# Optimization experiments

Hardware: AMD Instinct MI355X
Metric: run time of the kernel (lower is better)

## Reference

```python
import jax, jax.numpy as jnp
import numpy as np

N_NODES = 50000
N_EDGES = 800000
IN_FEATS = 256
OUT_FEATS = 128


def setup_inputs() -> dict:
    key = jax.random.key(0)
    k1, k2, k3, k4 = jax.random.split(key, 4)
    feat = jax.random.normal(k1, (N_NODES, IN_FEATS), dtype=jnp.float32)
    # xavier uniform init for weight [in, out]
    limit = float(np.sqrt(6.0 / (IN_FEATS + OUT_FEATS)))
    weight = jax.random.uniform(k2, (IN_FEATS, OUT_FEATS), minval=-limit, maxval=limit, dtype=jnp.float32)
    bias = jnp.zeros((OUT_FEATS,), dtype=jnp.float32)
    src = jax.random.randint(k3, (N_EDGES,), 0, N_NODES, dtype=jnp.int32)
    dst = jax.random.randint(k4, (N_EDGES,), 0, N_NODES, dtype=jnp.int32)
    return {"feat": feat, "weight": weight, "bias": bias, "src": src, "dst": dst}


def reference(feat, weight, bias, src, dst):
    N = feat.shape[0]
    in_f, out_f = weight.shape
    # right normalization: 1 / out_degree(src node), clamped to >= 1
    deg = jax.ops.segment_sum(jnp.ones(src.shape[0], dtype=feat.dtype), src, num_segments=N)
    norm = (1.0 / jnp.maximum(deg, 1.0))[:, None]  # [N,1]
    if in_f > out_f:
        # transform first (cheaper messages), then normalize + aggregate
        h = jnp.matmul(feat, weight) * norm          # [N, out]
        rst = jax.ops.segment_sum(h[src], dst, num_segments=N)  # scatter-sum over edges
    else:
        h = feat * norm                               # [N, in]
        rst = jax.ops.segment_sum(h[src], dst, num_segments=N)
        rst = jnp.matmul(rst, weight)
    return rst + bias
```

## Files before the change

kernel.cpp:

```cpp
#include <hip/hip_runtime.h>

#define N_NODES 50000
#define N_EDGES 800000
#define IN_F 256
#define OUT_F 128

#define CHUNKS 128
#define EPC (N_EDGES / CHUNKS)
#define BINW (N_NODES / 4)
#define NWORDS (N_NODES / 4)
#define RGB 196
#define HIST_BLOCKS (2 * CHUNKS)
#define CPW (CHUNKS / 4)

#define GEMM_START HIST_BLOCKS
#define GEMMF_BLOCKS 196
#define SCAT_BLOCKS 782

typedef __attribute__((ext_vector_type(8))) short short8;
typedef __attribute__((ext_vector_type(4))) float float4_t;

__device__ __forceinline__ short f2bf(float f) {
  unsigned u = __builtin_bit_cast(unsigned, f);
  u = u + 0x7FFFu + ((u >> 16) & 1u);
  return (short)(u >> 16);
}

__device__ __forceinline__ float bflo(unsigned u) {
  return __builtin_bit_cast(float, u << 16);
}
__device__ __forceinline__ float bfhi(unsigned u) {
  return __builtin_bit_cast(float, u & 0xFFFF0000u);
}

__global__ __launch_bounds__(512) void fused1_kernel(const int* __restrict__ src,
                                                     const int* __restrict__ dst,
                                                     unsigned char* __restrict__ pdst8,
                                                     unsigned char* __restrict__ psrc8,
                                                     unsigned char* __restrict__ rank8,
                                                     const float* __restrict__ W,
                                                     const float* __restrict__ feat,
                                                     unsigned short* __restrict__ h,
                                                     int* __restrict__ cursor) {
  __shared__ uint4 smem4[4096];
  int b = blockIdx.x;
  int tid = threadIdx.x;

  if (b >= GEMM_START) {
    if (b == GEMM_START && tid == 0) *cursor = 0;
    short* wl = (short*)smem4;
#pragma unroll
    for (int i = 0; i < 64; ++i) {
      int idx = i * 512 + tid;
      int k = idx >> 7, n = idx & 127;
      int s = k >> 5, q = (k >> 3) & 3, j = k & 7;
      int tt = n >> 4, m = n & 15;
      wl[((s * 8 + tt) * 64 + q * 16 + m) * 8 + j] = f2bf(W[idx]);
    }
    __syncthreads();

    int w = tid >> 6, l = tid & 63;
    int m = l & 15, q = l >> 4;
    long base = (long)(b - GEMM_START) * 256 + w * 32;

    float4_t acc[2][8];
#pragma unroll
    for (int r = 0; r < 2; ++r)
#pragma unroll
      for (int to = 0; to < 8; ++to) acc[r][to] = (float4_t)(0.0f);

    long row0 = base + m;
    long row1 = base + 16 + m;
    long r0c = row0 < N_NODES - 1 ? row0 : N_NODES - 1;
    long r1c = row1 < N_NODES - 1 ? row1 : N_NODES - 1;
    const float* a0p = feat + (size_t)r0c * IN_F;
    const float* a1p = feat + (size_t)r1c * IN_F;
    const short8* wl8 = (const short8*)smem4;

#pragma unroll
    for (int s = 0; s < 8; ++s) {
      int k0 = s * 32 + q * 8;
      float4_t av0a = *(const float4_t*)(a0p + k0);
      float4_t av0b = *(const float4_t*)(a0p + k0 + 4);
      float4_t av1a = *(const float4_t*)(a1p + k0);
      float4_t av1b = *(const float4_t*)(a1p + k0 + 4);
      short8 fa0, fa1;
#pragma unroll
      for (int i = 0; i < 4; ++i) {
        fa0[i] = f2bf(av0a[i]);
        fa0[i + 4] = f2bf(av0b[i]);
        fa1[i] = f2bf(av1a[i]);
        fa1[i + 4] = f2bf(av1b[i]);
      }
#pragma unroll
      for (int to = 0; to < 8; ++to) {
        short8 fb = wl8[(s * 8 + to) * 64 + l];
        acc[0][to] = __builtin_amdgcn_mfma_f32_16x16x32_bf16(fa0, fb, acc[0][to], 0, 0, 0);
        acc[1][to] = __builtin_amdgcn_mfma_f32_16x16x32_bf16(fa1, fb, acc[1][to], 0, 0, 0);
      }
    }

#pragma unroll
    for (int r = 0; r < 2; ++r) {
#pragma unroll
      for (int i = 0; i < 4; ++i) {
        long row = base + r * 16 + q * 4 + i;
        if (row < N_NODES) {
          size_t ho = (size_t)row * OUT_F;
#pragma unroll
          for (int to = 0; to < 8; ++to) {
            h[ho + to * 16 + m] = (unsigned short)f2bf(acc[r][to][i]);
          }
        }
      }
    }
    return;
  }

  unsigned* bins = (unsigned*)smem4;
  int hs = b >> 7;
  int c = b & 127;
  uint4* b4 = (uint4*)bins;
  for (int j = tid; j < BINW / 4; j += 512) b4[j] = (uint4){0u, 0u, 0u, 0u};
  __syncthreads();
  const int* key = hs ? src : dst;
  int e0 = c * EPC;

  auto process = [&](int v, int eI) {
    unsigned sh = (v & 3) * 8;
    unsigned old = atomicAdd(&bins[v >> 2], 1u << sh);
    if (!hs) rank8[eI] = (unsigned char)((old >> sh) & 0xFFu);
  };

#pragma unroll 2
  for (int tile = 0; tile < 3; ++tile) {
    int i = tile * 2048 + tid;
    int k0 = key[e0 + i];
    int k1 = key[e0 + i + 512];
    int k2 = key[e0 + i + 1024];
    int k3 = key[e0 + i + 1536];
    process(k0, e0 + i);
    process(k1, e0 + i + 512);
    process(k2, e0 + i + 1024);
    process(k3, e0 + i + 1536);
  }
  {
    int i = 6144 + tid;
    if (i < EPC) process(key[e0 + i], e0 + i);
  }
  __syncthreads();
  uint4* p128 = (uint4*)((hs ? psrc8 : pdst8) + (size_t)c * N_NODES);
  const uint4* s128 = (const uint4*)bins;
  for (int j = tid; j < BINW / 4; j += 512) p128[j] = s128[j];
}

__global__ __launch_bounds__(256) void reduceoff_kernel(const unsigned char* __restrict__ pdst8,
                                                        const unsigned char* __restrict__ psrc8,
                                                        unsigned char* __restrict__ delta8,
                                                        int* __restrict__ cnt,
                                                        int* __restrict__ row_start,
                                                        int* __restrict__ cursor,
                                                        float* __restrict__ norm) {
  __shared__ unsigned tot[4][64];
  int g = blockIdx.x, side = blockIdx.y;
  int t = threadIdx.x;
  int w = t >> 6, l = t & 63;
  int wd = g * 64 + l;
  bool ok = wd < NWORDS;
  int wdc = ok ? wd : NWORDS - 1;
  const unsigned* P = (const unsigned*)(side == 0 ? pdst8 : psrc8);

  unsigned vals[CPW];
  unsigned s = 0;
#pragma unroll
  for (int i = 0; i < CPW; ++i) {
    vals[i] = P[(size_t)(w * CPW + i) * NWORDS + wdc];
    s += vals[i];
  }
  tot[w][l] = s;
  __syncthreads();

  if (side == 0) {
    unsigned base = 0;
#pragma unroll
    for (int w2 = 0; w2 < 4; ++w2)
      if (w2 < w) base += tot[w2][l];
    unsigned run = base;
    unsigned* D = (unsigned*)delta8;
    if (ok) {
#pragma unroll
      for (int i = 0; i < CPW; ++i) {
        D[(size_t)(w * CPW + i) * NWORDS + wd] = run;
        run += vals[i];
      }
    }
    if (w == 0) {
      unsigned ftot = tot[0][l] + tot[1][l] + tot[2][l] + tot[3][l];
      if (!ok) ftot = 0;
      int c0 = ftot & 255, c1 = (ftot >> 8) & 255, c2 = (ftot >> 16) & 255, c3 = ftot >> 24;
      int T = c0 + c1 + c2 + c3;
      int x = T;
#pragma unroll
      for (int off = 1; off < 64; off <<= 1) {
        int y = __shfl_up(x, off);
        if (l >= off) x += y;
      }
      int waveTotal = __shfl(x, 63);
      int sb = 0;
      if (l == 63) sb = atomicAdd(cursor, waveTotal);
      sb = __shfl(sb, 63);
      int E = sb + x - T;
      if (ok) {
        int4 cv = {c0, c1, c2, c3};
        int4 rv = {E, E + c0, E + c0 + c1, E + c0 + c1 + c2};
        ((int4*)cnt)[wd] = cv;
        ((int4*)row_start)[wd] = rv;
      }
    }
  } else {
    if (w == 0 && ok) {
      unsigned ftot = tot[0][l] + tot[1][l] + tot[2][l] + tot[3][l];
      float4 nv;
      int d0 = ftot & 255, d1 = (ftot >> 8) & 255, d2 = (ftot >> 16) & 255, d3 = (int)(ftot >> 24);
      nv.x = 1.0f / (float)(d0 > 1 ? d0 : 1);
      nv.y = 1.0f / (float)(d1 > 1 ? d1 : 1);
      nv.z = 1.0f / (float)(d2 > 1 ? d2 : 1);
      nv.w = 1.0f / (float)(d3 > 1 ? d3 : 1);
      ((float4*)norm)[wd] = nv;
    }
  }
}

__global__ __launch_bounds__(256) void scat_kernel(const int* __restrict__ src,
                                                   const int* __restrict__ dst,
                                                   const int* __restrict__ row_start,
                                                   const unsigned char* __restrict__ delta8,
                                                   const unsigned char* __restrict__ rank8,
                                                   int* __restrict__ eidx) {
  int gt = blockIdx.x * 256 + threadIdx.x;
  int e = gt * 4;
  if (e >= N_EDGES) return;
  int4 d4 = *(const int4*)(dst + e);
  int4 s4 = *(const int4*)(src + e);
  unsigned rr = *(const unsigned*)(rank8 + e);
  int dd[4] = {d4.x, d4.y, d4.z, d4.w};
  int ss[4] = {s4.x, s4.y, s4.z, s4.w};
#pragma unroll
  for (int k = 0; k < 4; ++k) {
    int c = (e + k) / EPC;
    int d = dd[k];
    int pos = row_start[d] + (int)delta8[(size_t)c * N_NODES + d] + (int)((rr >> (8 * k)) & 0xFFu);
    eidx[pos] = ss[k];
  }
}

__global__ __launch_bounds__(256) void agg_kernel(const unsigned short* __restrict__ h,
                                                  const int* __restrict__ row_start,
                                                  const int* __restrict__ cnt,
                                                  const int* __restrict__ eidx,
                                                  const float* __restrict__ norm,
                                                  const float* __restrict__ bias,
                                                  float* __restrict__ out) {
  int w = threadIdx.x >> 6, l = threadIdx.x & 63;
  int d = blockIdx.x * 4 + w;
  int rs = row_start[d], re = rs + cnt[d];
  const unsigned* __restrict__ hu = (const unsigned*)h;
  int rowsel = l >> 5, cp = l & 31;
  float a0 = 0.f, a1 = 0.f, a2 = 0.f, a3 = 0.f;
  for (int bse = rs; bse < re; bse += 64) {
    int n = re - bse; if (n > 64) n = 64;
    int e = (l < n) ? eidx[bse + l] : 0;
    int half = (n + 1) >> 1;
    int j = 0;
    for (; j + 4 <= half; j += 4) {
      int i0 = 2 * j + rowsel;
      int s0 = __shfl(e, i0);
      int s1 = __shfl(e, i0 + 2);
      int s2 = __shfl(e, i0 + 4);
      int s3 = __shfl(e, i0 + 6);
      uint2 v0 = *(const uint2*)(hu + (size_t)s0 * 64 + 2 * cp);
      uint2 v1 = *(const uint2*)(hu + (size_t)s1 * 64 + 2 * cp);
      uint2 v2 = *(const uint2*)(hu + (size_t)s2 * 64 + 2 * cp);
      uint2 v3 = *(const uint2*)(hu + (size_t)s3 * 64 + 2 * cp);
      float nm0 = norm[s0], nm1 = norm[s1], nm2 = norm[s2], nm3 = norm[s3];
      if (i0 >= n) { v0.x = 0; v0.y = 0; }
      if (i0 + 2 >= n) { v1.x = 0; v1.y = 0; }
      if (i0 + 4 >= n) { v2.x = 0; v2.y = 0; }
      if (i0 + 6 >= n) { v3.x = 0; v3.y = 0; }
      a0 = fmaf(bflo(v0.x), nm0, a0); a1 = fmaf(bfhi(v0.x), nm0, a1);
      a2 = fmaf(bflo(v0.y), nm0, a2); a3 = fmaf(bfhi(v0.y), nm0, a3);
      a0 = fmaf(bflo(v1.x), nm1, a0); a1 = fmaf(bfhi(v1.x), nm1, a1);
      a2 = fmaf(bflo(v1.y), nm1, a2); a3 = fmaf(bfhi(v1.y), nm1, a3);
      a0 = fmaf(bflo(v2.x), nm2, a0); a1 = fmaf(bfhi(v2.x), nm2, a1);
      a2 = fmaf(bflo(v2.y), nm2, a2); a3 = fmaf(bfhi(v2.y), nm2, a3);
      a0 = fmaf(bflo(v3.x), nm3, a0); a1 = fmaf(bfhi(v3.x), nm3, a1);
      a2 = fmaf(bflo(v3.y), nm3, a2); a3 = fmaf(bfhi(v3.y), nm3, a3);
    }
    for (; j + 2 <= half; j += 2) {
      int i0 = 2 * j + rowsel;
      int i1 = i0 + 2;
      int s0 = __shfl(e, i0);
      int s1 = __shfl(e, i1);
      uint2 v0 = *(const uint2*)(hu + (size_t)s0 * 64 + 2 * cp);
      uint2 v1 = *(const uint2*)(hu + (size_t)s1 * 64 + 2 * cp);
      float nm0 = norm[s0], nm1 = norm[s1];
      if (i0 >= n) { v0.x = 0; v0.y = 0; }
      if (i1 >= n) { v1.x = 0; v1.y = 0; }
      a0 = fmaf(bflo(v0.x), nm0, a0); a1 = fmaf(bfhi(v0.x), nm0, a1);
      a2 = fmaf(bflo(v0.y), nm0, a2); a3 = fmaf(bfhi(v0.y), nm0, a3);
      a0 = fmaf(bflo(v1.x), nm1, a0); a1 = fmaf(bfhi(v1.x), nm1, a1);
      a2 = fmaf(bflo(v1.y), nm1, a2); a3 = fmaf(bfhi(v1.y), nm1, a3);
    }
    for (; j < half; ++j) {
      int i0 = 2 * j + rowsel;
      int s0 = __shfl(e, i0);
      uint2 v0 = *(const uint2*)(hu + (size_t)s0 * 64 + 2 * cp);
      float nm0 = norm[s0];
      if (i0 >= n) { v0.x = 0; v0.y = 0; }
      a0 = fmaf(bflo(v0.x), nm0, a0); a1 = fmaf(bfhi(v0.x), nm0, a1);
      a2 = fmaf(bflo(v0.y), nm0, a2); a3 = fmaf(bfhi(v0.y), nm0, a3);
    }
  }
  a0 += __shfl_xor(a0, 32);
  a1 += __shfl_xor(a1, 32);
  a2 += __shfl_xor(a2, 32);
  a3 += __shfl_xor(a3, 32);
  if (rowsel == 0) {
    float4 bv = ((const float4*)bias)[cp];
    float4 o;
    o.x = a0 + bv.x; o.y = a1 + bv.y; o.z = a2 + bv.z; o.w = a3 + bv.w;
    ((float4*)(out + (size_t)d * OUT_F))[cp] = o;
  }
}

extern "C" void kernel_launch(void* const* d_in, const int* in_sizes, int n_in,
                              void* d_out, int out_size, void* d_ws, size_t ws_size,
                              hipStream_t stream) {
  const float* feat = (const float*)d_in[0];
  const float* weight = (const float*)d_in[1];
  const float* bias = (const float*)d_in[2];
  const int* src = (const int*)d_in[3];
  const int* dst = (const int*)d_in[4];
  float* out = (float*)d_out;

  char* ws = (char*)d_ws;
  size_t off = 0;
  auto alloc = [&](size_t bytes) -> void* {
    void* p = ws + off;
    off += (bytes + 511) & ~(size_t)511;
    return p;
  };
  int* cursor = (int*)alloc(4);
  int* cnt = (int*)alloc(N_NODES * 4);
  int* row_start = (int*)alloc(N_NODES * 4);
  float* norm = (float*)alloc(N_NODES * 4);
  int* eidx = (int*)alloc(N_EDGES * 4);
  unsigned short* h = (unsigned short*)alloc((size_t)N_NODES * OUT_F * 2);
  unsigned char* pdst8 = (unsigned char*)alloc((size_t)CHUNKS * N_NODES);
  unsigned char* psrc8 = (unsigned char*)alloc((size_t)CHUNKS * N_NODES);
  unsigned char* delta8 = (unsigned char*)alloc((size_t)CHUNKS * N_NODES);
  unsigned char* rank8 = (unsigned char*)alloc((size_t)N_EDGES);
  (void)off; (void)ws_size; (void)in_sizes; (void)n_in; (void)out_size;

  hipLaunchKernelGGL(fused1_kernel, dim3(HIST_BLOCKS + GEMMF_BLOCKS), dim3(512), 0, stream,
                     src, dst, pdst8, psrc8, rank8, weight, feat, h, cursor);
  hipLaunchKernelGGL(reduceoff_kernel, dim3(RGB, 2), dim3(256), 0, stream,
                     pdst8, psrc8, delta8, cnt, row_start, cursor, norm);
  hipLaunchKernelGGL(scat_kernel, dim3(SCAT_BLOCKS), dim3(256), 0, stream,
                     src, dst, row_start, delta8, rank8, eidx);
  hipLaunchKernelGGL(agg_kernel, dim3(N_NODES / 4), dim3(256), 0, stream,
                     h, row_start, cnt, eidx, norm, bias, out);
}
```

Baseline: 170.7 us.

## Split aggregation columns across four grid-y blocks per destination node

The aggregation kernel now launches four blocks per group of destination nodes, each handling a quarter of the output columns (32 floats), with 16 lanes per edge row and four edge rows per wave step. The aim is more parallelism and more loads in flight per node. In exchange, each gather becomes a 64-byte segment per source row instead of 128 bytes. Edge indices and norm values are re-read four times, and per-lane loads shrink from 8 to 4 bytes.

```diff
diff --git a/kernel.cpp b/kernel.cpp
--- a/kernel.cpp
+++ b/kernel.cpp
@@ -263,73 +263,56 @@
                                                   float* __restrict__ out) {
   int w = threadIdx.x >> 6, l = threadIdx.x & 63;
   int d = blockIdx.x * 4 + w;
+  int cq = blockIdx.y;
   int rs = row_start[d], re = rs + cnt[d];
   const unsigned* __restrict__ hu = (const unsigned*)h;
-  int rowsel = l >> 5, cp = l & 31;
-  float a0 = 0.f, a1 = 0.f, a2 = 0.f, a3 = 0.f;
+  int rowsel = l >> 4;
+  int cp = l & 15;
+  int cbase = cq * 16;
+  float a0 = 0.f, a1 = 0.f;
   for (int bse = rs; bse < re; bse += 64) {
     int n = re - bse; if (n > 64) n = 64;
     int e = (l < n) ? eidx[bse + l] : 0;
-    int half = (n + 1) >> 1;
+    int quarter = (n + 3) >> 2;
     int j = 0;
-    for (; j + 4 <= half; j += 4) {
-      int i0 = 2 * j + rowsel;
+    for (; j + 4 <= quarter; j += 4) {
+      int i0 = 4 * j + rowsel;
       int s0 = __shfl(e, i0);
-      int s1 = __shfl(e, i0 + 2);
-      int s2 = __shfl(e, i0 + 4);
-      int s3 = __shfl(e, i0 + 6);
-      uint2 v0 = *(const uint2*)(hu + (size_t)s0 * 64 + 2 * cp);
-      uint2 v1 = *(const uint2*)(hu + (size_t)s1 * 64 + 2 * cp);
-      uint2 v2 = *(const uint2*)(hu + (size_t)s2 * 64 + 2 * cp);
-      uint2 v3 = *(const uint2*)(hu + (size_t)s3 * 64 + 2 * cp);
+      int s1 = __shfl(e, i0 + 4);
+      int s2 = __shfl(e, i0 + 8);
+      int s3 = __shfl(e, i0 + 12);
+      unsigned v0 = hu[(size_t)s0 * 64 + cbase + cp];
+      unsigned v1 = hu[(size_t)s1 * 64 + cbase + cp];
+      unsigned v2 = hu[(size_t)s2 * 64 + cbase + cp];
+      unsigned v3 = hu[(size_t)s3 * 64 + cbase + cp];
       float nm0 = norm[s0], nm1 = norm[s1], nm2 = norm[s2], nm3 = norm[s3];
-      if (i0 >= n) { v0.x = 0; v0.y = 0; }
-      if (i0 + 2 >= n) { v1.x = 0; v1.y = 0; }
-      if (i0 + 4 >= n) { v2.x = 0; v2.y = 0; }
-      if (i0 + 6 >= n) { v3.x = 0; v3.y = 0; }
-      a0 = fmaf(bflo(v0.x), nm0, a0); a1 = fmaf(bfhi(v0.x), nm0, a1);
-      a2 = fmaf(bflo(v0.y), nm0, a2); a3 = fmaf(bfhi(v0.y), nm0, a3);
-      a0 = fmaf(bflo(v1.x), nm1, a0); a1 = fmaf(bfhi(v1.x), nm1, a1);
-      a2 = fmaf(bflo(v1.y), nm1, a2); a3 = fmaf(bfhi(v1.y), nm1, a3);
-      a0 = fmaf(bflo(v2.x), nm2, a0); a1 = fmaf(bfhi(v2.x), nm2, a1);
-      a2 = fmaf(bflo(v2.y), nm2, a2); a3 = fmaf(bfhi(v2.y), nm2, a3);
-      a0 = fmaf(bflo(v3.x), nm3, a0); a1 = fmaf(bfhi(v3.x), nm3, a1);
-      a2 = fmaf(bflo(v3.y), nm3, a2); a3 = fmaf(bfhi(v3.y), nm3, a3);
-    }
-    for (; j + 2 <= half; j += 2) {
-      int i0 = 2 * j + rowsel;
-      int i1 = i0 + 2;
+      if (i0 >= n) v0 = 0u;
+      if (i0 + 4 >= n) v1 = 0u;
+      if (i0 + 8 >= n) v2 = 0u;
+      if (i0 + 12 >= n) v3 = 0u;
+      a0 = fmaf(bflo(v0), nm0, a0); a1 = fmaf(bfhi(v0), nm0, a1);
+      a0 = fmaf(bflo(v1), nm1, a0); a1 = fmaf(bfhi(v1), nm1, a1);
+      a0 = fmaf(bflo(v2), nm2, a0); a1 = fmaf(bfhi(v2), nm2, a1);
+      a0 = fmaf(bflo(v3), nm3, a0); a1 = fmaf(bfhi(v3), nm3, a1);
+    }
+    for (; j < quarter; ++j) {
+      int i0 = 4 * j + rowsel;
       int s0 = __shfl(e, i0);
-      int s1 = __shfl(e, i1);
-      uint2 v0 = *(const uint2*)(hu + (size_t)s0 * 64 + 2 * cp);
-      uint2 v1 = *(const uint2*)(hu + (size_t)s1 * 64 + 2 * cp);
-      float nm0 = norm[s0], nm1 = norm[s1];
-      if (i0 >= n) { v0.x = 0; v0.y = 0; }
-      if (i1 >= n) { v1.x = 0; v1.y = 0; }
-      a0 = fmaf(bflo(v0.x), nm0, a0); a1 = fmaf(bfhi(v0.x), nm0, a1);
-      a2 = fmaf(bflo(v0.y), nm0, a2); a3 = fmaf(bfhi(v0.y), nm0, a3);
-      a0 = fmaf(bflo(v1.x), nm1, a0); a1 = fmaf(bfhi(v1.x), nm1, a1);
-      a2 = fmaf(bflo(v1.y), nm1, a2); a3 = fmaf(bfhi(v1.y), nm1, a3);
-    }
-    for (; j < half; ++j) {
-      int i0 = 2 * j + rowsel;
-      int s0 = __shfl(e, i0);
-      uint2 v0 = *(const uint2*)(hu + (size_t)s0 * 64 + 2 * cp);
+      unsigned v0 = hu[(size_t)s0 * 64 + cbase + cp];
       float nm0 = norm[s0];
-      if (i0 >= n) { v0.x = 0; v0.y = 0; }
-      a0 = fmaf(bflo(v0.x), nm0, a0); a1 = fmaf(bfhi(v0.x), nm0, a1);
-      a2 = fmaf(bflo(v0.y), nm0, a2); a3 = fmaf(bfhi(v0.y), nm0, a3);
-    }
-  }
-  a0 += __shfl_xor(a0, 32);
-  a1 += __shfl_xor(a1, 32);
-  a2 += __shfl_xor(a2, 32);
-  a3 += __shfl_xor(a3, 32);
+      if (i0 >= n) v0 = 0u;
+      a0 = fmaf(bflo(v0), nm0, a0); a1 = fmaf(bfhi(v0), nm0, a1);
+    }
+  }
+  a0 += __shfl_xor(a0, 16); a1 += __shfl_xor(a1, 16);
+  a0 += __shfl_xor(a0, 32); a1 += __shfl_xor(a1, 32);
   if (rowsel == 0) {
-    float4 bv = ((const float4*)bias)[cp];
-    float4 o;
-    o.x = a0 + bv.x; o.y = a1 + bv.y; o.z = a2 + bv.z; o.w = a3 + bv.w;
-    ((float4*)(out + (size_t)d * OUT_F))[cp] = o;
+    int col = cbase * 2 + 2 * cp;
+    float2 bv = *(const float2*)(bias + col);
+    float2 o;
+    o.x = a0 + bv.x;
+    o.y = a1 + bv.y;
+    *(float2*)(out + (size_t)d * OUT_F + col) = o;
   }
 }
 
@@ -368,6 +351,6 @@
                      pdst8, psrc8, delta8, cnt, row_start, cursor, norm);
   hipLaunchKernelGGL(scat_kernel, dim3(SCAT_BLOCKS), dim3(256), 0, stream,
                      src, dst, row_start, delta8, rank8, eidx);
-  hipLaunchKernelGGL(agg_kernel, dim3(N_NODES / 4), dim3(256), 0, stream,
+  hipLaunchKernelGGL(agg_kernel, dim3(N_NODES / 4, 4), dim3(256), 0, stream,
                      h, row_start, cnt, eidx, norm, bias, out);
 }
```

Result: slower. 212.1 us (+24.3%).

## Replace chunked LDS histograms with global atomic counts and atomic-cursor scatter

Applied to the files above, without the earlier changes.

Replaces the per-chunk shared-memory byte histograms, the per-chunk partial-count arrays and their reduce/offset pass with direct global atomic degree counting, done in the same launch as the GEMM. Scatter now claims CSR slots with an atomicAdd on a per-node cursor instead of computing deterministic positions from rank and delta arrays. This removes roughly 38 MB of partial-histogram traffic but adds a zeroing kernel, contention on global atomics, and a nondeterministic edge order within each row, which can change the floating-point summation order.

```diff
diff --git a/kernel.cpp b/kernel.cpp
--- a/kernel.cpp
+++ b/kernel.cpp
@@ -4,18 +4,12 @@
 #define N_EDGES 800000
 #define IN_F 256
 #define OUT_F 128
-
-#define CHUNKS 128
-#define EPC (N_EDGES / CHUNKS)
-#define BINW (N_NODES / 4)
 #define NWORDS (N_NODES / 4)
-#define RGB 196
-#define HIST_BLOCKS (2 * CHUNKS)
-#define CPW (CHUNKS / 4)
-
-#define GEMM_START HIST_BLOCKS
+
 #define GEMMF_BLOCKS 196
+#define HISTB 391
 #define SCAT_BLOCKS 782
+#define ZERO_BLOCKS 13
 
 typedef __attribute__((ext_vector_type(8))) short short8;
 typedef __attribute__((ext_vector_type(4))) float float4_t;
@@ -33,21 +27,29 @@
   return __builtin_bit_cast(float, u & 0xFFFF0000u);
 }
 
+__global__ __launch_bounds__(1024) void zero_kernel(int* __restrict__ dstcnt,
+                                                    int* __restrict__ srccnt,
+                                                    int* __restrict__ cursor) {
+  int i = blockIdx.x * 1024 + threadIdx.x;
+  if (i == 0) *cursor = 0;
+  if (i < NWORDS) {
+    ((int4*)dstcnt)[i] = (int4){0, 0, 0, 0};
+    ((int4*)srccnt)[i] = (int4){0, 0, 0, 0};
+  }
+}
+
 __global__ __launch_bounds__(512) void fused1_kernel(const int* __restrict__ src,
                                                      const int* __restrict__ dst,
-                                                     unsigned char* __restrict__ pdst8,
-                                                     unsigned char* __restrict__ psrc8,
-                                                     unsigned char* __restrict__ rank8,
+                                                     int* __restrict__ dstcnt,
+                                                     int* __restrict__ srccnt,
                                                      const float* __restrict__ W,
                                                      const float* __restrict__ feat,
-                                                     unsigned short* __restrict__ h,
-                                                     int* __restrict__ cursor) {
+                                                     unsigned short* __restrict__ h) {
   __shared__ uint4 smem4[4096];
   int b = blockIdx.x;
   int tid = threadIdx.x;
 
-  if (b >= GEMM_START) {
-    if (b == GEMM_START && tid == 0) *cursor = 0;
+  if (b < GEMMF_BLOCKS) {
     short* wl = (short*)smem4;
 #pragma unroll
     for (int i = 0; i < 64; ++i) {
@@ -61,7 +63,7 @@
 
     int w = tid >> 6, l = tid & 63;
     int m = l & 15, q = l >> 4;
-    long base = (long)(b - GEMM_START) * 256 + w * 32;
+    long base = (long)b * 256 + w * 32;
 
     float4_t acc[2][8];
 #pragma unroll
@@ -117,139 +119,71 @@
     return;
   }
 
-  unsigned* bins = (unsigned*)smem4;
-  int hs = b >> 7;
-  int c = b & 127;
-  uint4* b4 = (uint4*)bins;
-  for (int j = tid; j < BINW / 4; j += 512) b4[j] = (uint4){0u, 0u, 0u, 0u};
-  __syncthreads();
-  const int* key = hs ? src : dst;
-  int e0 = c * EPC;
-
-  auto process = [&](int v, int eI) {
-    unsigned sh = (v & 3) * 8;
-    unsigned old = atomicAdd(&bins[v >> 2], 1u << sh);
-    if (!hs) rank8[eI] = (unsigned char)((old >> sh) & 0xFFu);
-  };
-
-#pragma unroll 2
-  for (int tile = 0; tile < 3; ++tile) {
-    int i = tile * 2048 + tid;
-    int k0 = key[e0 + i];
-    int k1 = key[e0 + i + 512];
-    int k2 = key[e0 + i + 1024];
-    int k3 = key[e0 + i + 1536];
-    process(k0, e0 + i);
-    process(k1, e0 + i + 512);
-    process(k2, e0 + i + 1024);
-    process(k3, e0 + i + 1536);
-  }
-  {
-    int i = 6144 + tid;
-    if (i < EPC) process(key[e0 + i], e0 + i);
-  }
-  __syncthreads();
-  uint4* p128 = (uint4*)((hs ? psrc8 : pdst8) + (size_t)c * N_NODES);
-  const uint4* s128 = (const uint4*)bins;
-  for (int j = tid; j < BINW / 4; j += 512) p128[j] = s128[j];
-}
-
-__global__ __launch_bounds__(256) void reduceoff_kernel(const unsigned char* __restrict__ pdst8,
-                                                        const unsigned char* __restrict__ psrc8,
-                                                        unsigned char* __restrict__ delta8,
-                                                        int* __restrict__ cnt,
-                                                        int* __restrict__ row_start,
-                                                        int* __restrict__ cursor,
-                                                        float* __restrict__ norm) {
-  __shared__ unsigned tot[4][64];
-  int g = blockIdx.x, side = blockIdx.y;
-  int t = threadIdx.x;
-  int w = t >> 6, l = t & 63;
-  int wd = g * 64 + l;
-  bool ok = wd < NWORDS;
-  int wdc = ok ? wd : NWORDS - 1;
-  const unsigned* P = (const unsigned*)(side == 0 ? pdst8 : psrc8);
-
-  unsigned vals[CPW];
-  unsigned s = 0;
-#pragma unroll
-  for (int i = 0; i < CPW; ++i) {
-    vals[i] = P[(size_t)(w * CPW + i) * NWORDS + wdc];
-    s += vals[i];
-  }
-  tot[w][l] = s;
-  __syncthreads();
-
-  if (side == 0) {
-    unsigned base = 0;
-#pragma unroll
-    for (int w2 = 0; w2 < 4; ++w2)
-      if (w2 < w) base += tot[w2][l];
-    unsigned run = base;
-    unsigned* D = (unsigned*)delta8;
-    if (ok) {
-#pragma unroll
-      for (int i = 0; i < CPW; ++i) {
-        D[(size_t)(w * CPW + i) * NWORDS + wd] = run;
-        run += vals[i];
-      }
-    }
-    if (w == 0) {
-      unsigned ftot = tot[0][l] + tot[1][l] + tot[2][l] + tot[3][l];
-      if (!ok) ftot = 0;
-      int c0 = ftot & 255, c1 = (ftot >> 8) & 255, c2 = (ftot >> 16) & 255, c3 = ftot >> 24;
-      int T = c0 + c1 + c2 + c3;
-      int x = T;
-#pragma unroll
-      for (int off = 1; off < 64; off <<= 1) {
-        int y = __shfl_up(x, off);
-        if (l >= off) x += y;
-      }
-      int waveTotal = __shfl(x, 63);
-      int sb = 0;
-      if (l == 63) sb = atomicAdd(cursor, waveTotal);
-      sb = __shfl(sb, 63);
-      int E = sb + x - T;
-      if (ok) {
-        int4 cv = {c0, c1, c2, c3};
-        int4 rv = {E, E + c0, E + c0 + c1, E + c0 + c1 + c2};
-        ((int4*)cnt)[wd] = cv;
-        ((int4*)row_start)[wd] = rv;
-      }
-    }
-  } else {
-    if (w == 0 && ok) {
-      unsigned ftot = tot[0][l] + tot[1][l] + tot[2][l] + tot[3][l];
-      float4 nv;
-      int d0 = ftot & 255, d1 = (ftot >> 8) & 255, d2 = (ftot >> 16) & 255, d3 = (int)(ftot >> 24);
-      nv.x = 1.0f / (float)(d0 > 1 ? d0 : 1);
-      nv.y = 1.0f / (float)(d1 > 1 ? d1 : 1);
-      nv.z = 1.0f / (float)(d2 > 1 ? d2 : 1);
-      nv.w = 1.0f / (float)(d3 > 1 ? d3 : 1);
-      ((float4*)norm)[wd] = nv;
-    }
-  }
-}
-
-__global__ __launch_bounds__(256) void scat_kernel(const int* __restrict__ src,
-                                                   const int* __restrict__ dst,
-                                                   const int* __restrict__ row_start,
-                                                   const unsigned char* __restrict__ delta8,
-                                                   const unsigned char* __restrict__ rank8,
-                                                   int* __restrict__ eidx) {
-  int gt = blockIdx.x * 256 + threadIdx.x;
-  int e = gt * 4;
+  int hb = b - GEMMF_BLOCKS;
+  int e = hb * 2048 + tid * 4;
   if (e >= N_EDGES) return;
   int4 d4 = *(const int4*)(dst + e);
   int4 s4 = *(const int4*)(src + e);
-  unsigned rr = *(const unsigned*)(rank8 + e);
+  atomicAdd(&dstcnt[d4.x], 1);
+  atomicAdd(&dstcnt[d4.y], 1);
+  atomicAdd(&dstcnt[d4.z], 1);
+  atomicAdd(&dstcnt[d4.w], 1);
+  atomicAdd(&srccnt[s4.x], 1);
+  atomicAdd(&srccnt[s4.y], 1);
+  atomicAdd(&srccnt[s4.z], 1);
+  atomicAdd(&srccnt[s4.w], 1);
+}
+
+__global__ __launch_bounds__(256) void alloc_kernel(const int* __restrict__ dstcnt,
+                                                    const int* __restrict__ srccnt,
+                                                    int* __restrict__ row_start,
+                                                    int* __restrict__ cur,
+                                                    float* __restrict__ norm,
+                                                    int* __restrict__ cursor) {
+  int tid = threadIdx.x;
+  int w = tid >> 6, l = tid & 63;
+  int wd = (blockIdx.x * 4 + w) * 64 + l;
+  bool ok = wd < NWORDS;
+  int4 c4 = ok ? ((const int4*)dstcnt)[wd] : (int4){0, 0, 0, 0};
+  int T = c4.x + c4.y + c4.z + c4.w;
+  int x = T;
+#pragma unroll
+  for (int off = 1; off < 64; off <<= 1) {
+    int y = __shfl_up(x, off);
+    if (l >= off) x += y;
+  }
+  int waveTotal = __shfl(x, 63);
+  int sb = 0;
+  if (l == 63) sb = atomicAdd(cursor, waveTotal);
+  sb = __shfl(sb, 63);
+  int E = sb + x - T;
+  if (ok) {
+    int4 rv = {E, E + c4.x, E + c4.x + c4.y, E + c4.x + c4.y + c4.z};
+    ((int4*)row_start)[wd] = rv;
+    ((int4*)cur)[wd] = rv;
+    int4 s4v = ((const int4*)srccnt)[wd];
+    float4 nv;
+    nv.x = 1.0f / (float)(s4v.x > 1 ? s4v.x : 1);
+    nv.y = 1.0f / (float)(s4v.y > 1 ? s4v.y : 1);
+    nv.z = 1.0f / (float)(s4v.z > 1 ? s4v.z : 1);
+    nv.w = 1.0f / (float)(s4v.w > 1 ? s4v.w : 1);
+    ((float4*)norm)[wd] = nv;
+  }
+}
+
+__global__ __launch_bounds__(256) void scat_kernel(const int* __restrict__ src,
+                                                   const int* __restrict__ dst,
+                                                   int* __restrict__ cur,
+                                                   int* __restrict__ eidx) {
+  int e = (blockIdx.x * 256 + threadIdx.x) * 4;
+  if (e >= N_EDGES) return;
+  int4 d4 = *(const int4*)(dst + e);
+  int4 s4 = *(const int4*)(src + e);
   int dd[4] = {d4.x, d4.y, d4.z, d4.w};
   int ss[4] = {s4.x, s4.y, s4.z, s4.w};
 #pragma unroll
   for (int k = 0; k < 4; ++k) {
-    int c = (e + k) / EPC;
-    int d = dd[k];
-    int pos = row_start[d] + (int)delta8[(size_t)c * N_NODES + d] + (int)((rr >> (8 * k)) & 0xFFu);
+    int pos = atomicAdd(&cur[dd[k]], 1);
     eidx[pos] = ss[k];
   }
 }
@@ -351,23 +285,23 @@
     return p;
   };
   int* cursor = (int*)alloc(4);
-  int* cnt = (int*)alloc(N_NODES * 4);
+  int* dstcnt = (int*)alloc(N_NODES * 4);
+  int* srccnt = (int*)alloc(N_NODES * 4);
   int* row_start = (int*)alloc(N_NODES * 4);
+  int* cur = (int*)alloc(N_NODES * 4);
   float* norm = (float*)alloc(N_NODES * 4);
   int* eidx = (int*)alloc(N_EDGES * 4);
   unsigned short* h = (unsigned short*)alloc((size_t)N_NODES * OUT_F * 2);
-  unsigned char* pdst8 = (unsigned char*)alloc((size_t)CHUNKS * N_NODES);
-  unsigned char* psrc8 = (unsigned char*)alloc((size_t)CHUNKS * N_NODES);
-  unsigned char* delta8 = (unsigned char*)alloc((size_t)CHUNKS * N_NODES);
-  unsigned char* rank8 = (unsigned char*)alloc((size_t)N_EDGES);
   (void)off; (void)ws_size; (void)in_sizes; (void)n_in; (void)out_size;
 
-  hipLaunchKernelGGL(fused1_kernel, dim3(HIST_BLOCKS + GEMMF_BLOCKS), dim3(512), 0, stream,
-                     src, dst, pdst8, psrc8, rank8, weight, feat, h, cursor);
-  hipLaunchKernelGGL(reduceoff_kernel, dim3(RGB, 2), dim3(256), 0, stream,
-                     pdst8, psrc8, delta8, cnt, row_start, cursor, norm);
+  hipLaunchKernelGGL(zero_kernel, dim3(ZERO_BLOCKS), dim3(1024), 0, stream,
+                     dstcnt, srccnt, cursor);
+  hipLaunchKernelGGL(fused1_kernel, dim3(GEMMF_BLOCKS + HISTB), dim3(512), 0, stream,
+                     src, dst, dstcnt, srccnt, weight, feat, h);
+  hipLaunchKernelGGL(alloc_kernel, dim3(49), dim3(256), 0, stream,
+                     dstcnt, srccnt, row_start, cur, norm, cursor);
   hipLaunchKernelGGL(scat_kernel, dim3(SCAT_BLOCKS), dim3(256), 0, stream,
-                     src, dst, row_start, delta8, rank8, eidx);
+                     src, dst, cur, eidx);
   hipLaunchKernelGGL(agg_kernel, dim3(N_NODES / 4), dim3(256), 0, stream,
-                     h, row_start, cnt, eidx, norm, bias, out);
-}
+                     h, row_start, dstcnt, eidx, norm, bias, out);
+}
```

Result: slower. 246.3 us (+44.3%).
